# Kernel optimization log

Hardware: AMD Instinct MI355X
Metric: run time of the kernel (lower is better)

## Reference

```python
import jax, jax.numpy as jnp
import numpy as np

NO, NR, E, D = 50000, 2000, 600000, 128
NEG_SLOPE = 0.2


def setup_inputs() -> dict:
    key = jax.random.key(0)
    ks = jax.random.split(key, 16)
    p = lambda k, shape: jax.random.normal(k, shape, dtype=jnp.float32) * 0.05
    return {
        "x_order": jax.random.normal(ks[0], (NO, D), dtype=jnp.float32),
        "x_rider": jax.random.normal(ks[1], (NR, D), dtype=jnp.float32),
        "order_idx": jax.random.randint(ks[2], (E,), 0, NO),
        "rider_idx": jax.random.randint(ks[3], (E,), 0, NR),
        # GATConv layer 1 (order_input_dim=128 -> hidden_dim=128, heads=1)
        "Ws1": p(ks[4], (D, D)), "Wd1": p(ks[5], (D, D)),
        "as1": p(ks[6], (D,)), "ad1": p(ks[7], (D,)), "b1": jnp.zeros((D,), jnp.float32),
        # GATConv layer 2 (hidden_dim=128 -> output_dim=128, heads=1)
        "Ws2": p(ks[8], (D, D)), "Wd2": p(ks[9], (D, D)),
        "as2": p(ks[10], (D,)), "ad2": p(ks[11], (D,)), "b2": jnp.zeros((D,), jnp.float32),
    }


def _segment_softmax(e, seg, num_segments):
    # numerically-stable softmax over edges grouped by destination node
    m = jax.ops.segment_max(e, seg, num_segments=num_segments)
    ex = jnp.exp(e - m[seg])
    s = jax.ops.segment_sum(ex, seg, num_segments=num_segments)
    return ex / (s[seg] + 1e-16)


def _gat_bipartite(x_src, x_dst, oi, ri, Ws, Wd, a_src, a_dst, b, n_dst):
    # PyG GATConv, heads=1, bipartite (src=order, dst=rider), no self-loops
    hs = x_src @ Ws            # [NO, D]
    hd = x_dst @ Wd            # [NR, D]
    alpha_s = hs @ a_src       # [NO]
    alpha_d = hd @ a_dst       # [NR]
    e = jax.nn.leaky_relu(alpha_s[oi] + alpha_d[ri], NEG_SLOPE)  # [E]
    alpha = _segment_softmax(e, ri, n_dst)                        # [E]
    out = jax.ops.segment_sum(alpha[:, None] * hs[oi], ri, num_segments=n_dst)
    return out + b


def reference(x_order, x_rider, order_idx, rider_idx,
              Ws1, Wd1, as1, ad1, b1, Ws2, Wd2, as2, ad2, b2):
    n_rider = x_rider.shape[0]
    # layer 1: update riders; order features pass through
    r1 = jax.nn.relu(_gat_bipartite(x_order, x_rider, order_idx, rider_idx,
                                    Ws1, Wd1, as1, ad1, b1, n_rider))
    o1 = jax.nn.relu(x_order)
    # layer 2
    r2 = _gat_bipartite(o1, r1, order_idx, rider_idx,
                        Ws2, Wd2, as2, ad2, b2, n_rider)
    # per-edge gather-dot-sigmoid scoring
    scores = jnp.sum(o1[order_idx] * r2[rider_idx], axis=1)
    return jax.nn.sigmoid(scores)
```

## Files before the change

### kernel.cpp

```cpp
#include <hip/hip_runtime.h>
#include <hip/hip_fp16.h>
#include <math.h>

#define NO 50000
#define NR 2000
#define NE 600000
#define D  128
#define NEG_SLOPE 0.2f
#define CAP 512
#define NB 256
#define CH ((NE + NB - 1) / NB)

__global__ void precompute_wv(const float* __restrict__ Ws1, const float* __restrict__ as1,
                              const float* __restrict__ Wd1, const float* __restrict__ ad1,
                              const float* __restrict__ Ws2, const float* __restrict__ as2,
                              const float* __restrict__ Wd2, const float* __restrict__ ad2,
                              float* __restrict__ wsv1, float* __restrict__ wdv1,
                              float* __restrict__ wsv2, float* __restrict__ wdv2) {
    int k = threadIdx.x;
    float s1 = 0.f, d1 = 0.f, s2 = 0.f, d2 = 0.f;
    for (int j = 0; j < D; ++j) {
        s1 += Ws1[k * D + j] * as1[j];
        d1 += Wd1[k * D + j] * ad1[j];
        s2 += Ws2[k * D + j] * as2[j];
        d2 += Wd2[k * D + j] * ad2[j];
    }
    wsv1[k] = s1; wdv1[k] = d1; wsv2[k] = s2; wdv2[k] = d2;
}

__global__ void order_prep(const float* __restrict__ x,
                           const float* __restrict__ wsv1, const float* __restrict__ wsv2,
                           float* __restrict__ as1o, float* __restrict__ as2o,
                           __half* __restrict__ x16, __half* __restrict__ xr16) {
    int wave = (blockIdx.x * blockDim.x + threadIdx.x) >> 6;
    int lane = threadIdx.x & 63;
    if (wave >= NO) return;
    float2 xv = ((const float2*)(x + (size_t)wave * D))[lane];
    float2 w1 = ((const float2*)wsv1)[lane];
    float2 w2 = ((const float2*)wsv2)[lane];
    float rx0 = fmaxf(xv.x, 0.f), rx1 = fmaxf(xv.y, 0.f);
    ((__half2*)(x16  + (size_t)wave * D))[lane] = __floats2half2_rn(xv.x, xv.y);
    ((__half2*)(xr16 + (size_t)wave * D))[lane] = __floats2half2_rn(rx0, rx1);
    float a1 = xv.x * w1.x + xv.y * w1.y;
    float a2 = rx0 * w2.x + rx1 * w2.y;
    for (int off = 32; off; off >>= 1) {
        a1 += __shfl_down(a1, off);
        a2 += __shfl_down(a2, off);
    }
    if (lane == 0) { as1o[wave] = a1; as2o[wave] = a2; }
}

__global__ void rider_alpha(const float* __restrict__ xr, const float* __restrict__ wdv1,
                            float* __restrict__ ad1r) {
    int wave = (blockIdx.x * blockDim.x + threadIdx.x) >> 6;
    int lane = threadIdx.x & 63;
    if (wave >= NR) return;
    const float* row = xr + (size_t)wave * D;
    float a = row[lane] * wdv1[lane] + row[lane + 64] * wdv1[lane + 64];
    for (int off = 32; off; off >>= 1) a += __shfl_down(a, off);
    if (lane == 0) ad1r[wave] = a;
}


__global__ void blockhist_kernel(const int* __restrict__ ri, int* __restrict__ blockHist) {
    __shared__ int h[NR];
    int b = blockIdx.x, t = threadIdx.x;
    for (int i = t; i < NR; i += 256) h[i] = 0;
    __syncthreads();
    int lo = b * CH;
    int hi = lo + CH; if (hi > NE) hi = NE;
    for (int i = lo + t; i < hi; i += 256) atomicAdd(&h[ri[i]], 1);
    __syncthreads();
    for (int i = t; i < NR; i += 256) blockHist[(size_t)b * NR + i] = h[i];
}

__global__ void rowscan_kernel(int* __restrict__ blockHist, int* __restrict__ total) {
    int r = blockIdx.x * blockDim.x + threadIdx.x;
    if (r >= NR) return;
    int run = 0;
    for (int b = 0; b < NB; ++b) {
        int idx = b * NR + r;
        int v = blockHist[idx];
        blockHist[idx] = run;
        run += v;
    }
    total[r] = run;
}

__global__ void scan_kernel(const int* __restrict__ total, int* __restrict__ starts) {
    __shared__ int sums[256];
    int t = threadIdx.x;
    int v[8];
    int s = 0;
    for (int j = 0; j < 8; ++j) {
        int idx = t * 8 + j;
        int c = (idx < NR) ? total[idx] : 0;
        v[j] = s;
        s += c;
    }
    sums[t] = s;
    __syncthreads();
    for (int off = 1; off < 256; off <<= 1) {
        int add = (t >= off) ? sums[t - off] : 0;
        __syncthreads();
        sums[t] += add;
        __syncthreads();
    }
    int base = sums[t] - s;
    for (int j = 0; j < 8; ++j) {
        int idx = t * 8 + j;
        if (idx < NR) starts[idx] = base + v[j];
    }
}

__global__ void scatter_kernel(const int* __restrict__ oi, const int* __restrict__ ri,
                               const int* __restrict__ starts,
                               const int* __restrict__ blockHist,
                               int* __restrict__ sOrd) {
    __shared__ int h[NR];
    int b = blockIdx.x, t = threadIdx.x;
    for (int i = t; i < NR; i += 256) h[i] = 0;
    __syncthreads();
    int lo = b * CH;
    int hi = lo + CH; if (hi > NE) hi = NE;
    for (int i = lo + t; i < hi; i += 256) {
        int r = ri[i];
        int rank = atomicAdd(&h[r], 1);
        int pos = starts[r] + blockHist[(size_t)b * NR + r] + rank;
        sOrd[pos] = oi[i];
    }
}

template <int L>
__global__ void rider_agg(const __half* __restrict__ xg, const float* __restrict__ as_o,
                          const float* __restrict__ ad_r,
                          const int* __restrict__ starts, const int* __restrict__ cnt,
                          const int* __restrict__ sOrd,
                          const float* __restrict__ W, const float* __restrict__ bias,
                          const float* __restrict__ wdv2,
                          float* __restrict__ ad2r, __half* __restrict__ r216) {
    __shared__ float eL[CAP];
    __shared__ int   sO[CAP];
    __shared__ float red[256];
    __shared__ float red8[256][9];
    __shared__ float tl[D];
    int r = blockIdx.x;
    int t = threadIdx.x;
    int base = starts[r], n = cnt[r];
    float ad = ad_r[r];

    float lmax = -1e30f;
    for (int i = t; i < n; i += 256) {
        int o = sOrd[base + i];
        float e = as_o[o] + ad;
        e = (e > 0.f) ? e : NEG_SLOPE * e;
        if (i < CAP) { eL[i] = e; sO[i] = o; }
        lmax = fmaxf(lmax, e);
    }
    red[t] = lmax;
    __syncthreads();
    for (int off = 128; off; off >>= 1) {
        if (t < off) red[t] = fmaxf(red[t], red[t + off]);
        __syncthreads();
    }
    float m = red[0];
    __syncthreads();

    float ls = 0.f;
    for (int i = t; i < n; i += 256) {
        float e;
        if (i < CAP) e = eL[i];
        else {
            int o = sOrd[base + i];
            e = as_o[o] + ad;
            e = (e > 0.f) ? e : NEG_SLOPE * e;
        }
        float ex = __expf(e - m);
        if (i < CAP) eL[i] = ex;
        ls += ex;
    }
    red[t] = ls;
    __syncthreads();
    for (int off = 128; off; off >>= 1) {
        if (t < off) red[t] += red[t + off];
        __syncthreads();
    }
    float inv = 1.f / (red[0] + 1e-16f);
    __syncthreads();

    int grp = t >> 4;
    int lh  = t & 15;
    float acc[8];
#pragma unroll
    for (int k = 0; k < 8; ++k) acc[k] = 0.f;
    for (int i = grp; i < n; i += 16) {
        float a; int o;
        if (i < CAP) { a = eL[i]; o = sO[i]; }
        else {
            o = sOrd[base + i];
            float e = as_o[o] + ad;
            e = (e > 0.f) ? e : NEG_SLOPE * e;
            a = __expf(e - m);
        }
        uint4 hv = ((const uint4*)(xg + (size_t)o * D))[lh];
        float2 f0 = __half22float2(*(const __half2*)&hv.x);
        float2 f1 = __half22float2(*(const __half2*)&hv.y);
        float2 f2 = __half22float2(*(const __half2*)&hv.z);
        float2 f3 = __half22float2(*(const __half2*)&hv.w);
        acc[0] += a * f0.x; acc[1] += a * f0.y;
        acc[2] += a * f1.x; acc[3] += a * f1.y;
        acc[4] += a * f2.x; acc[5] += a * f2.y;
        acc[6] += a * f3.x; acc[7] += a * f3.y;
    }
#pragma unroll
    for (int k = 0; k < 8; ++k) red8[t][k] = acc[k];
    __syncthreads();
    if (t < D) {
        int lh2 = t >> 3, k = t & 7;
        float s = 0.f;
        for (int g = 0; g < 16; ++g) s += red8[g * 16 + lh2][k];
        tl[t] = s * inv;
    }
    __syncthreads();

    int d = t & 127, h = t >> 7;
    float acc2 = 0.f;
    for (int k = h * 64; k < h * 64 + 64; ++k) acc2 += tl[k] * W[k * D + d];
    red[t] = acc2;
    __syncthreads();
    if (L == 1) {
        if (t < 128) red[t] = fmaxf(red[t] + red[t + 128] + bias[t], 0.f) * wdv2[t];
        __syncthreads();
        for (int off = 64; off; off >>= 1) {
            if (t < off) red[t] += red[t + off];
            __syncthreads();
        }
        if (t == 0) ad2r[r] = red[0];
    } else {
        if (t < 128) r216[(size_t)r * D + t] = __float2half(red[t] + red[t + 128] + bias[t]);
    }
}

__global__ void score_edges(const __half* __restrict__ xr16, const __half* __restrict__ r216,
                            const int* __restrict__ oi, const int* __restrict__ ri,
                            float* __restrict__ out) {
    int gid = blockIdx.x * blockDim.x + threadIdx.x;
    int e  = gid >> 4;
    int lh = gid & 15;
    if (e >= NE) return;
    int o = oi[e], r = ri[e];
    uint4 hx = ((const uint4*)(xr16 + (size_t)o * D))[lh];
    uint4 hr = ((const uint4*)(r216 + (size_t)r * D))[lh];
    float2 a0 = __half22float2(*(const __half2*)&hx.x);
    float2 a1 = __half22float2(*(const __half2*)&hx.y);
    float2 a2 = __half22float2(*(const __half2*)&hx.z);
    float2 a3 = __half22float2(*(const __half2*)&hx.w);
    float2 b0 = __half22float2(*(const __half2*)&hr.x);
    float2 b1 = __half22float2(*(const __half2*)&hr.y);
    float2 b2 = __half22float2(*(const __half2*)&hr.z);
    float2 b3 = __half22float2(*(const __half2*)&hr.w);
    float p = a0.x * b0.x + a0.y * b0.y + a1.x * b1.x + a1.y * b1.y +
              a2.x * b2.x + a2.y * b2.y + a3.x * b3.x + a3.y * b3.y;
    p += __shfl_xor(p, 8);
    p += __shfl_xor(p, 4);
    p += __shfl_xor(p, 2);
    p += __shfl_xor(p, 1);
    if (lh == 0) out[e] = 1.f / (1.f + __expf(-p));
}

extern "C" void kernel_launch(void* const* d_in, const int* in_sizes, int n_in,
                              void* d_out, int out_size, void* d_ws, size_t ws_size,
                              hipStream_t stream) {
    const float* x_order = (const float*)d_in[0];
    const float* x_rider = (const float*)d_in[1];
    const int*   oi      = (const int*)d_in[2];
    const int*   ri      = (const int*)d_in[3];
    const float* Ws1 = (const float*)d_in[4];
    const float* Wd1 = (const float*)d_in[5];
    const float* as1 = (const float*)d_in[6];
    const float* ad1 = (const float*)d_in[7];
    const float* b1  = (const float*)d_in[8];
    const float* Ws2 = (const float*)d_in[9];
    const float* Wd2 = (const float*)d_in[10];
    const float* as2 = (const float*)d_in[11];
    const float* ad2 = (const float*)d_in[12];
    const float* b2  = (const float*)d_in[13];
    float* out = (float*)d_out;

    char* w = (char*)d_ws;
    float* wsv1 = (float*)w; w += 512;
    float* wdv1 = (float*)w; w += 512;
    float* wsv2 = (float*)w; w += 512;
    float* wdv2 = (float*)w; w += 512;
    float* as1o = (float*)w; w += (size_t)NO * 4;
    float* as2o = (float*)w; w += (size_t)NO * 4;
    float* ad1r = (float*)w; w += (size_t)NR * 4;
    float* ad2r = (float*)w; w += (size_t)NR * 4;
    int* total  = (int*)w;   w += (size_t)NR * 4;
    int* starts = (int*)w;   w += (size_t)NR * 4;
    int* blockHist = (int*)w; w += (size_t)NB * NR * 4;
    int* sOrd   = (int*)w;   w += (size_t)NE * 4;
    __half* x16  = (__half*)w; w += (size_t)NO * D * 2;
    __half* xr16 = (__half*)w; w += (size_t)NO * D * 2;
    __half* r216 = (__half*)w; w += (size_t)NR * D * 2;

    precompute_wv<<<1, 128, 0, stream>>>(Ws1, as1, Wd1, ad1, Ws2, as2, Wd2, ad2,
                                         wsv1, wdv1, wsv2, wdv2);
    order_prep<<<NO / 4, 256, 0, stream>>>(x_order, wsv1, wsv2, as1o, as2o, x16, xr16);
    rider_alpha<<<NR / 4, 256, 0, stream>>>(x_rider, wdv1, ad1r);

    blockhist_kernel<<<NB, 256, 0, stream>>>(ri, blockHist);
    rowscan_kernel<<<(NR + 255) / 256, 256, 0, stream>>>(blockHist, total);
    scan_kernel<<<1, 256, 0, stream>>>(total, starts);
    scatter_kernel<<<NB, 256, 0, stream>>>(oi, ri, starts, blockHist, sOrd);

    rider_agg<1><<<NR, 256, 0, stream>>>(x16, as1o, ad1r, starts, total, sOrd,
                                         Ws1, b1, wdv2, ad2r, ((__half*)0));
    rider_agg<2><<<NR, 256, 0, stream>>>(xr16, as2o, ad2r, starts, total, sOrd,
                                         Ws2, b2, wdv2, (float*)0, r216);
    score_edges<<<(NE * 16 + 255) / 256, 256, 0, stream>>>(xr16, r216, oi, ri, out);
}
```

Measured before the change: 242.1 us.

## Drop relu fp16 copy, merge prep kernels, skip softmax max pass

The separate relu'd fp16 copy of order features is removed, and relu is now applied on the fly in the layer-2 aggregation and the edge scoring. The order-prep and rider-alpha kernels are merged into one launch. The segment-softmax max-reduction pass is dropped, so exp(e) is used directly. This cuts a 12.8MB write plus a launch and a reduction phase, but drops numerical stabilisation, which relies on attention logits staying small. CAP is also lowered from 512 to 448.

After: 233.8 us. 1.04x faster.

```diff
diff --git a/kernel.cpp b/kernel.cpp
--- a/kernel.cpp
+++ b/kernel.cpp
@@ -7,7 +7,7 @@
 #define NE 600000
 #define D  128
 #define NEG_SLOPE 0.2f
-#define CAP 512
+#define CAP 448
 #define NB 256
 #define CH ((NE + NB - 1) / NB)
 
@@ -28,37 +28,34 @@
     wsv1[k] = s1; wdv1[k] = d1; wsv2[k] = s2; wdv2[k] = d2;
 }
 
-__global__ void order_prep(const float* __restrict__ x,
-                           const float* __restrict__ wsv1, const float* __restrict__ wsv2,
-                           float* __restrict__ as1o, float* __restrict__ as2o,
-                           __half* __restrict__ x16, __half* __restrict__ xr16) {
-    int wave = (blockIdx.x * blockDim.x + threadIdx.x) >> 6;
+__global__ void node_prep(const float* __restrict__ x, const float* __restrict__ xr,
+                          const float* __restrict__ wsv1, const float* __restrict__ wsv2,
+                          const float* __restrict__ wdv1,
+                          float* __restrict__ as1o, float* __restrict__ as2o,
+                          float* __restrict__ ad1r, __half* __restrict__ x16) {
     int lane = threadIdx.x & 63;
-    if (wave >= NO) return;
-    float2 xv = ((const float2*)(x + (size_t)wave * D))[lane];
-    float2 w1 = ((const float2*)wsv1)[lane];
-    float2 w2 = ((const float2*)wsv2)[lane];
-    float rx0 = fmaxf(xv.x, 0.f), rx1 = fmaxf(xv.y, 0.f);
-    ((__half2*)(x16  + (size_t)wave * D))[lane] = __floats2half2_rn(xv.x, xv.y);
-    ((__half2*)(xr16 + (size_t)wave * D))[lane] = __floats2half2_rn(rx0, rx1);
-    float a1 = xv.x * w1.x + xv.y * w1.y;
-    float a2 = rx0 * w2.x + rx1 * w2.y;
-    for (int off = 32; off; off >>= 1) {
-        a1 += __shfl_down(a1, off);
-        a2 += __shfl_down(a2, off);
-    }
-    if (lane == 0) { as1o[wave] = a1; as2o[wave] = a2; }
-}
-
-__global__ void rider_alpha(const float* __restrict__ xr, const float* __restrict__ wdv1,
-                            float* __restrict__ ad1r) {
-    int wave = (blockIdx.x * blockDim.x + threadIdx.x) >> 6;
-    int lane = threadIdx.x & 63;
-    if (wave >= NR) return;
-    const float* row = xr + (size_t)wave * D;
-    float a = row[lane] * wdv1[lane] + row[lane + 64] * wdv1[lane + 64];
-    for (int off = 32; off; off >>= 1) a += __shfl_down(a, off);
-    if (lane == 0) ad1r[wave] = a;
+    if (blockIdx.x < NO / 4) {
+        int row = blockIdx.x * 4 + (threadIdx.x >> 6);
+        float2 xv = ((const float2*)(x + (size_t)row * D))[lane];
+        float2 w1 = ((const float2*)wsv1)[lane];
+        float2 w2 = ((const float2*)wsv2)[lane];
+        float rx0 = fmaxf(xv.x, 0.f), rx1 = fmaxf(xv.y, 0.f);
+        ((__half2*)(x16 + (size_t)row * D))[lane] = __floats2half2_rn(xv.x, xv.y);
+        float a1 = xv.x * w1.x + xv.y * w1.y;
+        float a2 = rx0 * w2.x + rx1 * w2.y;
+        for (int off = 32; off; off >>= 1) {
+            a1 += __shfl_down(a1, off);
+            a2 += __shfl_down(a2, off);
+        }
+        if (lane == 0) { as1o[row] = a1; as2o[row] = a2; }
+    } else {
+        int row = (blockIdx.x - NO / 4) * 4 + (threadIdx.x >> 6);
+        float2 xv = ((const float2*)(xr + (size_t)row * D))[lane];
+        float2 w1 = ((const float2*)wdv1)[lane];
+        float a = xv.x * w1.x + xv.y * w1.y;
+        for (int off = 32; off; off >>= 1) a += __shfl_down(a, off);
+        if (lane == 0) ad1r[row] = a;
+    }
 }
 
 
@@ -132,7 +129,7 @@
 }
 
 template <int L>
-__global__ void rider_agg(const __half* __restrict__ xg, const float* __restrict__ as_o,
+__global__ void rider_agg(const __half* __restrict__ x16, const float* __restrict__ as_o,
                           const float* __restrict__ ad_r,
                           const int* __restrict__ starts, const int* __restrict__ cnt,
                           const int* __restrict__ sOrd,
@@ -144,39 +141,17 @@
     __shared__ float red[256];
     __shared__ float red8[256][9];
     __shared__ float tl[D];
-    int r = blockIdx.x;
-    int t = threadIdx.x;
+    int r = blockIdx.x, t = threadIdx.x;
     int base = starts[r], n = cnt[r];
     float ad = ad_r[r];
 
-    float lmax = -1e30f;
+    float ls = 0.f;
     for (int i = t; i < n; i += 256) {
         int o = sOrd[base + i];
         float e = as_o[o] + ad;
         e = (e > 0.f) ? e : NEG_SLOPE * e;
-        if (i < CAP) { eL[i] = e; sO[i] = o; }
-        lmax = fmaxf(lmax, e);
-    }
-    red[t] = lmax;
-    __syncthreads();
-    for (int off = 128; off; off >>= 1) {
-        if (t < off) red[t] = fmaxf(red[t], red[t + off]);
-        __syncthreads();
-    }
-    float m = red[0];
-    __syncthreads();
-
-    float ls = 0.f;
-    for (int i = t; i < n; i += 256) {
-        float e;
-        if (i < CAP) e = eL[i];
-        else {
-            int o = sOrd[base + i];
-            e = as_o[o] + ad;
-            e = (e > 0.f) ? e : NEG_SLOPE * e;
-        }
-        float ex = __expf(e - m);
-        if (i < CAP) eL[i] = ex;
+        float ex = __expf(e);
+        if (i < CAP) { eL[i] = ex; sO[i] = o; }
         ls += ex;
     }
     red[t] = ls;
@@ -188,8 +163,7 @@
     float inv = 1.f / (red[0] + 1e-16f);
     __syncthreads();
 
-    int grp = t >> 4;
-    int lh  = t & 15;
+    int grp = t >> 4, lh = t & 15;
     float acc[8];
 #pragma unroll
     for (int k = 0; k < 8; ++k) acc[k] = 0.f;
@@ -200,13 +174,19 @@
             o = sOrd[base + i];
             float e = as_o[o] + ad;
             e = (e > 0.f) ? e : NEG_SLOPE * e;
-            a = __expf(e - m);
+            a = __expf(e);
         }
-        uint4 hv = ((const uint4*)(xg + (size_t)o * D))[lh];
+        uint4 hv = ((const uint4*)(x16 + (size_t)o * D))[lh];
         float2 f0 = __half22float2(*(const __half2*)&hv.x);
         float2 f1 = __half22float2(*(const __half2*)&hv.y);
         float2 f2 = __half22float2(*(const __half2*)&hv.z);
         float2 f3 = __half22float2(*(const __half2*)&hv.w);
+        if (L == 2) {
+            f0.x = fmaxf(f0.x, 0.f); f0.y = fmaxf(f0.y, 0.f);
+            f1.x = fmaxf(f1.x, 0.f); f1.y = fmaxf(f1.y, 0.f);
+            f2.x = fmaxf(f2.x, 0.f); f2.y = fmaxf(f2.y, 0.f);
+            f3.x = fmaxf(f3.x, 0.f); f3.y = fmaxf(f3.y, 0.f);
+        }
         acc[0] += a * f0.x; acc[1] += a * f0.y;
         acc[2] += a * f1.x; acc[3] += a * f1.y;
         acc[4] += a * f2.x; acc[5] += a * f2.y;
@@ -224,9 +204,9 @@
     __syncthreads();
 
     int d = t & 127, h = t >> 7;
-    float acc2 = 0.f;
-    for (int k = h * 64; k < h * 64 + 64; ++k) acc2 += tl[k] * W[k * D + d];
-    red[t] = acc2;
+    float a2 = 0.f;
+    for (int k = h * 64; k < h * 64 + 64; ++k) a2 += tl[k] * W[k * D + d];
+    red[t] = a2;
     __syncthreads();
     if (L == 1) {
         if (t < 128) red[t] = fmaxf(red[t] + red[t + 128] + bias[t], 0.f) * wdv2[t];
@@ -241,7 +221,7 @@
     }
 }
 
-__global__ void score_edges(const __half* __restrict__ xr16, const __half* __restrict__ r216,
+__global__ void score_edges(const __half* __restrict__ x16, const __half* __restrict__ r216,
                             const int* __restrict__ oi, const int* __restrict__ ri,
                             float* __restrict__ out) {
     int gid = blockIdx.x * blockDim.x + threadIdx.x;
@@ -249,7 +229,7 @@
     int lh = gid & 15;
     if (e >= NE) return;
     int o = oi[e], r = ri[e];
-    uint4 hx = ((const uint4*)(xr16 + (size_t)o * D))[lh];
+    uint4 hx = ((const uint4*)(x16  + (size_t)o * D))[lh];
     uint4 hr = ((const uint4*)(r216 + (size_t)r * D))[lh];
     float2 a0 = __half22float2(*(const __half2*)&hx.x);
     float2 a1 = __half22float2(*(const __half2*)&hx.y);
@@ -259,8 +239,10 @@
     float2 b1 = __half22float2(*(const __half2*)&hr.y);
     float2 b2 = __half22float2(*(const __half2*)&hr.z);
     float2 b3 = __half22float2(*(const __half2*)&hr.w);
-    float p = a0.x * b0.x + a0.y * b0.y + a1.x * b1.x + a1.y * b1.y +
-              a2.x * b2.x + a2.y * b2.y + a3.x * b3.x + a3.y * b3.y;
+    float p = fmaxf(a0.x, 0.f) * b0.x + fmaxf(a0.y, 0.f) * b0.y +
+              fmaxf(a1.x, 0.f) * b1.x + fmaxf(a1.y, 0.f) * b1.y +
+              fmaxf(a2.x, 0.f) * b2.x + fmaxf(a2.y, 0.f) * b2.y +
+              fmaxf(a3.x, 0.f) * b3.x + fmaxf(a3.y, 0.f) * b3.y;
     p += __shfl_xor(p, 8);
     p += __shfl_xor(p, 4);
     p += __shfl_xor(p, 2);
@@ -301,13 +283,12 @@
     int* blockHist = (int*)w; w += (size_t)NB * NR * 4;
     int* sOrd   = (int*)w;   w += (size_t)NE * 4;
     __half* x16  = (__half*)w; w += (size_t)NO * D * 2;
-    __half* xr16 = (__half*)w; w += (size_t)NO * D * 2;
     __half* r216 = (__half*)w; w += (size_t)NR * D * 2;
 
     precompute_wv<<<1, 128, 0, stream>>>(Ws1, as1, Wd1, ad1, Ws2, as2, Wd2, ad2,
                                          wsv1, wdv1, wsv2, wdv2);
-    order_prep<<<NO / 4, 256, 0, stream>>>(x_order, wsv1, wsv2, as1o, as2o, x16, xr16);
-    rider_alpha<<<NR / 4, 256, 0, stream>>>(x_rider, wdv1, ad1r);
+    node_prep<<<NO / 4 + NR / 4, 256, 0, stream>>>(x_order, x_rider, wsv1, wsv2, wdv1,
+                                                   as1o, as2o, ad1r, x16);
 
     blockhist_kernel<<<NB, 256, 0, stream>>>(ri, blockHist);
     rowscan_kernel<<<(NR + 255) / 256, 256, 0, stream>>>(blockHist, total);
@@ -315,8 +296,8 @@
     scatter_kernel<<<NB, 256, 0, stream>>>(oi, ri, starts, blockHist, sOrd);
 
     rider_agg<1><<<NR, 256, 0, stream>>>(x16, as1o, ad1r, starts, total, sOrd,
-                                         Ws1, b1, wdv2, ad2r, ((__half*)0));
-    rider_agg<2><<<NR, 256, 0, stream>>>(xr16, as2o, ad2r, starts, total, sOrd,
-                                         Ws2, b2, wdv2, (float*)0, r216);
-    score_edges<<<(NE * 16 + 255) / 256, 256, 0, stream>>>(xr16, r216, oi, ri, out);
-}
+                                         Ws1, b1, wdv2, ad2r, (__half*)0);
+    rider_agg<2><<<NR, 256, 0, stream>>>(x16, as2o, ad2r, starts, total, sOrd,
+                                         Ws2, b2, (float*)0, (float*)0, r216);
+    score_edges<<<(NE * 16 + 255) / 256, 256, 0, stream>>>(x16, r216, oi, ri, out);
+}
```
